# Optimization experiments

Hardware: AMD Instinct MI355X
Metric: run time of the kernel (lower is better)

## Reference

```python
import jax, jax.numpy as jnp
import numpy as np

SEQ, B, V, D, H, R = 256, 64, 10000, 1024, 1024, 2


def setup_inputs() -> dict:
    key = jax.random.key(0)
    ks = jax.random.split(key, 8)
    s = 0.02
    return {
        "tokens": jax.random.randint(ks[0], (SEQ, B), 0, V),           # (seq, batch)
        "emb": jax.random.uniform(ks[1], (V, D), minval=-0.1, maxval=0.1),
        "qw": jax.random.normal(ks[2], (R, D, H)) * s,   # Qw: nhid -> ninp, per mogrify iter
        "qb": jnp.zeros((R, D)),
        "rw": jax.random.normal(ks[3], (R, H, D)) * s,   # Rw: ninp -> nhid
        "rb": jnp.zeros((R, H)),
        "w_ih": jax.random.normal(ks[4], (4 * H, D)) * s,
        "w_hh": jax.random.normal(ks[5], (4 * H, H)) * s,
        "b_ih": jnp.zeros((4 * H,)),
        "b_hh": jnp.zeros((4 * H,)),
        "dec_w": jax.random.uniform(ks[6], (V, H), minval=-0.1, maxval=0.1),
        "dec_b": jnp.zeros((V,)),
        "h0": jnp.zeros((B, H)),
        "c0": jnp.zeros((B, H)),
    }


def reference(tokens, emb, qw, qb, rw, rb, w_ih, w_hh, b_ih, b_hh, dec_w, dec_b, h0, c0):
    def step(carry, tok):
        h, c = carry                      # (B, H), (B, H)
        x = emb[tok]                      # embedding lookup -> (B, D)
        # Mogrify: R alternating gating iterations (dropout=0 / eval mode)
        for r_ in range(R):
            x = 2.0 * jax.nn.sigmoid(h @ qw[r_].T + qb[r_]) * x   # (B, D)
            h = 2.0 * jax.nn.sigmoid(x @ rw[r_].T + rb[r_]) * h   # (B, H)
        # single-layer LSTM cell (PyTorch gate order: i, f, g, o)
        gates = x @ w_ih.T + b_ih + h @ w_hh.T + b_hh              # (B, 4H)
        i, f, g, o = jnp.split(gates, 4, axis=-1)
        c_new = jax.nn.sigmoid(f) * c + jax.nn.sigmoid(i) * jnp.tanh(g)
        h_new = jax.nn.sigmoid(o) * jnp.tanh(c_new)
        dec = h_new @ dec_w.T + dec_b                              # (B, V)
        return (h_new, c_new), dec

    (h_f, c_f), decoded = jax.lax.scan(step, (h0, c0), tokens)     # decoded: (SEQ, B, V)
    return decoded, h_f, c_f
```

## Files before the change

kernel.cpp:

```cpp
#include <hip/hip_runtime.h>
#include <hip/hip_bf16.h>

#define SEQ_LEN 256
#define NB 64
#define NV 10000
#define NVP 10048
#define ND 1024
#define NBLK 256

typedef unsigned int u32;
typedef unsigned short u16;
typedef u32 u32x4 __attribute__((ext_vector_type(4)));
typedef short s16x8 __attribute__((ext_vector_type(8)));
typedef float f32x4 __attribute__((ext_vector_type(4)));

__device__ __forceinline__ float sigf(float z) { return 1.f / (1.f + expf(-z)); }

__device__ __forceinline__ float bflo(u32 u) {
  union { u32 i; float f; } v; v.i = u << 16; return v.f;
}
__device__ __forceinline__ float bfhi(u32 u) {
  union { u32 i; float f; } v; v.i = u & 0xffff0000u; return v.f;
}
__device__ __forceinline__ u16 f2bf(float f) {
  u32 u = __float_as_uint(f);
  u32 r = u + 0x7FFFu + ((u >> 16) & 1u);
  return (u16)(r >> 16);
}

__device__ __forceinline__ void st_uc1(u32* p, u32 v) {
  asm volatile("global_store_dword %0, %1, off sc1" :: "v"(p), "v"(v) : "memory");
}
__device__ __forceinline__ void ld_a4_issue(const u32* p, u32x4& a0, u32x4& a1,
                                            u32x4& a2, u32x4& a3) {
  asm volatile(
      "global_load_dwordx4 %0, %4, off sc1\n\t"
      "global_load_dwordx4 %1, %4, off offset:64 sc1\n\t"
      "global_load_dwordx4 %2, %4, off offset:128 sc1\n\t"
      "global_load_dwordx4 %3, %4, off offset:192 sc1"
      : "=&v"(a0), "=&v"(a1), "=&v"(a2), "=&v"(a3)
      : "v"(p)
      : "memory");
}
__device__ __forceinline__ void wait_vm0() {
  asm volatile("s_waitcnt vmcnt(0)" ::: "memory");
  __builtin_amdgcn_sched_barrier(0);
}
__device__ __forceinline__ s16x8 as_frag(u32x4 v) {
  union { u32x4 u; s16x8 s; } c; c.u = v; return c.s;
}

__device__ __forceinline__ float dot8_f32(const float* hv, const float* wp, float acc) {
  float4 w0 = *(const float4*)wp;
  float4 w1 = *(const float4*)(wp + 4);
  acc += hv[0] * w0.x; acc += hv[1] * w0.y; acc += hv[2] * w0.z; acc += hv[3] * w0.w;
  acc += hv[4] * w1.x; acc += hv[5] * w1.y; acc += hv[6] * w1.z; acc += hv[7] * w1.w;
  return acc;
}

__global__ void floodk(float* out, float val, unsigned long long n) {
  unsigned long long i = (unsigned long long)blockIdx.x * 256 + threadIdx.x;
  if (i < n) out[i] = val;
}

__global__ void init_state(const float* __restrict__ h0, const float* __restrict__ c0,
                           float* __restrict__ cS, u16* __restrict__ hx16, u32* flags) {
  int i = blockIdx.x * 256 + threadIdx.x;
  int k = i >> 6, b = i & 63;
  cS[i] = c0[b * ND + k];
  hx16[b * ND + k] = f2bf(h0[b * ND + k]);
  if (i < NBLK) flags[i] = 0u;
}

__global__ void cvt_dec(const float* __restrict__ decw, u16* __restrict__ Wb) {
  size_t i = (size_t)blockIdx.x * 256 + threadIdx.x;
  size_t base = i * 8;
  if (base >= (size_t)NVP * ND) return;
  size_t row = base >> 10;
  ushort4 o0, o1;
  if (row < NV) {
    float4 v0 = *(const float4*)(decw + base);
    float4 v1 = *(const float4*)(decw + base + 4);
    o0 = make_ushort4(f2bf(v0.x), f2bf(v0.y), f2bf(v0.z), f2bf(v0.w));
    o1 = make_ushort4(f2bf(v1.x), f2bf(v1.y), f2bf(v1.z), f2bf(v1.w));
  } else {
    o0 = make_ushort4(0, 0, 0, 0); o1 = o0;
  }
  *(ushort4*)(Wb + base) = o0;
  *(ushort4*)(Wb + base + 4) = o1;
}


__device__ __forceinline__ void fbar(u32* flags, u32 want) {
  asm volatile("s_waitcnt vmcnt(0)" ::: "memory");
  __syncthreads();
  const int tid = threadIdx.x;
  if (tid == 0)
    __hip_atomic_store(flags + blockIdx.x, want,
                       __ATOMIC_RELAXED, __HIP_MEMORY_SCOPE_AGENT);
  if (tid < 64) {
    const u32* fp = flags + tid * 4;
    for (;;) {
      u32x4 f;
      asm volatile("global_load_dwordx4 %0, %1, off sc1\n\ts_waitcnt vmcnt(0)"
                   : "=&v"(f) : "v"(fp) : "memory");
      int ok = (f[0] >= want) & (f[1] >= want) & (f[2] >= want) & (f[3] >= want);
      if (__all(ok)) break;
      __builtin_amdgcn_s_sleep(1);
    }
  }
  __syncthreads();
}

template<bool EMB>
__device__ __forceinline__ void mogP(
    const u32* __restrict__ actU, const u16* wAll, int rowbase, const float* bL,
    const float* __restrict__ emb, const int* __restrict__ tok,
    const u32* __restrict__ multU, u32* __restrict__ outU,
    float* red, float* vals2, float* vals)
{
  const int tid = threadIdx.x;
  const int wv = tid >> 6, lane = tid & 63;
  const int c0 = blockIdx.x * 4;
  const int kb = wv * 128;
  const int lm = lane & 15, lh = lane >> 4;
  const u32* ap = actU + (size_t)lm * 512 + (kb >> 1) + lh * 4;
  const int g = rowbase + lm;
  const int swz = (g & 7) << 3;

  u32x4 A[4][4];
#pragma unroll
  for (int m = 0; m < 4; ++m)
    ld_a4_issue(ap + m * 8192, A[m][0], A[m][1], A[m][2], A[m][3]);
  u32 mu = 0;
  if (!EMB && tid < 256) {
    const int ec = tid >> 6, eb = tid & 63;
    const u32* mp = multU + (size_t)eb * 512 + ((c0 + ec) >> 1);
    asm volatile("global_load_dword %0, %1, off sc1" : "=&v"(mu) : "v"(mp) : "memory");
  }
  s16x8 bf[4];
#pragma unroll
  for (int ks = 0; ks < 4; ++ks)
    bf[ks] = *(const s16x8*)(wAll + g * 1024 + ((kb + ks * 32 + lh * 8) ^ swz));
  wait_vm0();

  f32x4 acc[4];
#pragma unroll
  for (int m = 0; m < 4; ++m) { acc[m] = (f32x4){0.f,0.f,0.f,0.f}; }
#pragma unroll
  for (int ks = 0; ks < 4; ++ks)
#pragma unroll
    for (int m = 0; m < 4; ++m)
      acc[m] = __builtin_amdgcn_mfma_f32_16x16x32_bf16(as_frag(A[m][ks]), bf[ks], acc[m], 0, 0, 0);

#pragma unroll
  for (int m = 0; m < 4; ++m)
#pragma unroll
    for (int r = 0; r < 4; ++r)
      red[wv * 1024 + (m * 4 + r) * 64 + lane] = acc[m][r];
  __syncthreads();
  {
    float s0 = 0.f, s1 = 0.f;
#pragma unroll
    for (int w = 0; w < 8; ++w) { s0 += red[w * 1024 + tid]; s1 += red[w * 1024 + 512 + tid]; }
    vals2[tid] = s0; vals2[512 + tid] = s1;
  }
  __syncthreads();

  if (tid < 256) {
    const int c = tid >> 6, b = tid & 63;
    const int i = ((b >> 4) << 2) | (b & 3);
    const int l = (((b >> 2) & 3) << 4) | c;
    float z = vals2[i * 64 + l] + bL[c];
    float g2 = 2.f * sigf(z);
    float m;
    if (EMB) m = emb[(size_t)tok[b] * ND + (c0 + c)];
    else     m = (c & 1) ? bfhi(mu) : bflo(mu);
    vals[c * 64 + b] = g2 * m;
  }
  __syncthreads();

  if (tid < 128) {
    const int cp = tid >> 6, b = tid & 63;
    float lo = vals[(2 * cp) * 64 + b];
    float hi = vals[(2 * cp + 1) * 64 + b];
    u32 pk = (u32)f2bf(lo) | ((u32)f2bf(hi) << 16);
    st_uc1(outU + (size_t)b * 512 + (c0 >> 1) + cp, pk);
  }
}

__device__ __forceinline__ void gatesP(
    const u32* __restrict__ xU, const u32* __restrict__ hU,
    const u16* wAll, const float* bG, float& creg,
    u32* __restrict__ hBrow, u32* __restrict__ hxU, float* __restrict__ hFw,
    float* red, float* vals2, float* vals)
{
  const int tid = threadIdx.x;
  const int wv = tid >> 6, lane = tid & 63;
  const int j0 = blockIdx.x * 4;
  const int half = wv >> 2, kq = wv & 3;
  const int kb = kq * 256;
  const int lm = lane & 15, lh = lane >> 4;
  const u32* ap = (half ? hU : xU) + (size_t)lm * 512 + (kb >> 1) + lh * 4;
  const int g = 16 + half * 16 + lm;
  const int swz = (g & 7) << 3;

  u32x4 A[4][8];
#pragma unroll
  for (int m = 0; m < 4; ++m) {
    ld_a4_issue(ap + m * 8192,      A[m][0], A[m][1], A[m][2], A[m][3]);
    ld_a4_issue(ap + m * 8192 + 64, A[m][4], A[m][5], A[m][6], A[m][7]);
  }
  s16x8 bf[8];
#pragma unroll
  for (int ks = 0; ks < 8; ++ks)
    bf[ks] = *(const s16x8*)(wAll + g * 1024 + ((kb + ks * 32 + lh * 8) ^ swz));
  wait_vm0();

  f32x4 acc[4];
#pragma unroll
  for (int m = 0; m < 4; ++m) { acc[m] = (f32x4){0.f,0.f,0.f,0.f}; }
#pragma unroll
  for (int ks = 0; ks < 8; ++ks)
#pragma unroll
    for (int m = 0; m < 4; ++m)
      acc[m] = __builtin_amdgcn_mfma_f32_16x16x32_bf16(as_frag(A[m][ks]), bf[ks], acc[m], 0, 0, 0);

#pragma unroll
  for (int m = 0; m < 4; ++m)
#pragma unroll
    for (int r = 0; r < 4; ++r)
      red[wv * 1024 + (m * 4 + r) * 64 + lane] = acc[m][r];
  __syncthreads();
  {
    float s0 = 0.f, s1 = 0.f;
#pragma unroll
    for (int w = 0; w < 8; ++w) { s0 += red[w * 1024 + tid]; s1 += red[w * 1024 + 512 + tid]; }
    vals2[tid] = s0; vals2[512 + tid] = s1;
  }
  __syncthreads();

  if (tid < 256) {
    const int jj = tid >> 6, b = tid & 63;
    const int i = ((b >> 4) << 2) | (b & 3);
    const int lbase = (((b >> 2) & 3) << 4);
    float pre[4];
#pragma unroll
    for (int gg = 0; gg < 4; ++gg) {
      const int n = jj * 4 + gg;
      pre[gg] = vals2[i * 64 + (lbase | n)] + bG[n];
    }
    float iv = sigf(pre[0]), fv = sigf(pre[1]);
    float gv = tanhf(pre[2]), ov = sigf(pre[3]);
    float cn = fv * creg + iv * gv;
    creg = cn;
    float hn = ov * tanhf(cn);
    vals[jj * 64 + b] = hn;
    if (hFw) hFw[(size_t)(j0 + jj) * NB + b] = hn;
  }
  __syncthreads();

  if (tid < 128) {
    const int cp = tid >> 6, b = tid & 63;
    float lo = vals[(2 * cp) * 64 + b];
    float hi = vals[(2 * cp + 1) * 64 + b];
    u32 pk = (u32)f2bf(lo) | ((u32)f2bf(hi) << 16);
    st_uc1(hxU + (size_t)b * 512 + (blockIdx.x * 2) + cp, pk);
    hBrow[(size_t)b * 512 + (blockIdx.x * 2) + cp] = pk;
  }
}

__global__ __launch_bounds__(512) void seq_kernel(
    const int* __restrict__ tokens, const float* __restrict__ emb,
    const float* __restrict__ qw, const float* __restrict__ qb,
    const float* __restrict__ rw, const float* __restrict__ rb,
    const float* __restrict__ wih, const float* __restrict__ whh,
    const float* __restrict__ bih, const float* __restrict__ bhh,
    u32* __restrict__ hxU, u32* __restrict__ xAU, u32* __restrict__ h1U,
    u32* __restrict__ xBU, u32* __restrict__ h3U,
    float* __restrict__ cS, u32* __restrict__ hB, float* __restrict__ hF,
    u32* flags)
{
  __shared__ u16 wAll[48 * 1024];
  __shared__ float red[8 * 1024];
  __shared__ float vals2[1024];
  __shared__ float vals[256];
  __shared__ float bMog[4][4];
  __shared__ float bGs[16];

  const int tid = threadIdx.x;
  const int c0 = blockIdx.x * 4;
  const size_t DH = (size_t)ND * ND;

  {
    const float* msrc[4] = {qw, rw, qw + DH, rw + DH};
#pragma unroll
    for (int m = 0; m < 4; ++m)
      for (int c = 0; c < 4; ++c) {
        const int g = m * 4 + c;
        const float* src = msrc[m] + (size_t)(c0 + c) * ND;
        u16* dst = wAll + g * 1024;
        const int swz = (g & 7) << 3;
        for (int k = tid; k < ND; k += 512) dst[k ^ swz] = f2bf(src[k]);
      }
#pragma unroll
    for (int m = 0; m < 2; ++m) {
      const float* W = m ? whh : wih;
      for (int r = 0; r < 16; ++r) {
        const int g = 16 + m * 16 + r;
        const float* src = W + ((size_t)(r & 3) * ND + c0 + (r >> 2)) * ND;
        u16* dst = wAll + g * 1024;
        const int swz = (g & 7) << 3;
        for (int k = tid; k < ND; k += 512) dst[k ^ swz] = f2bf(src[k]);
      }
    }
    if (tid < 16) {
      int p = tid >> 2, c = tid & 3;
      const float* bs = (p == 0) ? qb : (p == 1) ? rb : (p == 2) ? qb + ND : rb + ND;
      bMog[p][c] = bs[c0 + c];
    }
    if (tid >= 16 && tid < 32) {
      int r = tid - 16;
      int jj = r >> 2, g = r & 3;
      bGs[r] = bih[g * ND + c0 + jj] + bhh[g * ND + c0 + jj];
    }
  }
  float creg = 0.f;
  if (tid < 256) creg = cS[(size_t)(c0 + (tid >> 6)) * NB + (tid & 63)];
  __syncthreads();

  u32 want = 0;
  for (int t = 0; t < SEQ_LEN; ++t) {
    const int* tok = tokens + (size_t)t * NB;
    u32* hBrow = hB + (size_t)t * 32768;
    float* hFw = (t == SEQ_LEN - 1) ? hF : nullptr;
    mogP<true >(hxU, wAll, 0,  bMog[0], emb, tok, nullptr, xAU, red, vals2, vals); fbar(flags, ++want);
    mogP<false>(xAU, wAll, 4,  bMog[1], nullptr, nullptr, hxU, h1U, red, vals2, vals); fbar(flags, ++want);
    mogP<false>(h1U, wAll, 8,  bMog[2], nullptr, nullptr, xAU, xBU, red, vals2, vals); fbar(flags, ++want);
    mogP<false>(xBU, wAll, 12, bMog[3], nullptr, nullptr, h1U, h3U, red, vals2, vals); fbar(flags, ++want);
    gatesP(xBU, h3U, wAll, bGs, creg, hBrow, hxU, hFw, red, vals2, vals);              fbar(flags, ++want);
  }
  if (tid < 256) cS[(size_t)(c0 + (tid >> 6)) * NB + (tid & 63)] = creg;
}

__global__ __launch_bounds__(256) void decode_mfma(
    const u32* __restrict__ hB,
    const u16* __restrict__ Wb,
    const float* __restrict__ bias,
    float* __restrict__ out)
{
  int bid = blockIdx.x;
  bid = (bid & 7) * (NBLK * 157 / 8) + (bid >> 3);
  const int mt = bid / 157;
  const int nt = bid % 157;
  const int tid = threadIdx.x;
  const int wv = tid >> 6, lane = tid & 63;
  const int lm = lane & 15, lh = lane >> 4;
  const int n = nt * 64 + wv * 16 + lm;
  const u16* bp = Wb + (size_t)n * 1024 + lh * 8;
  const u32* ap = hB + (size_t)mt * 32768 + (size_t)lm * 512 + lh * 4;

  f32x4 acc[4];
#pragma unroll
  for (int m = 0; m < 4; ++m) acc[m] = (f32x4){0.f, 0.f, 0.f, 0.f};

#pragma unroll 4
  for (int ks = 0; ks < 32; ++ks) {
    s16x8 bf = *(const s16x8*)(bp + ks * 32);
#pragma unroll
    for (int m = 0; m < 4; ++m) {
      u32x4 av = *(const u32x4*)(ap + m * 8192 + ks * 16);
      acc[m] = __builtin_amdgcn_mfma_f32_16x16x32_bf16(as_frag(av), bf, acc[m], 0, 0, 0);
    }
  }

  const float db = (n < NV) ? bias[n] : 0.f;
  float* orow = out + (size_t)mt * NB * NV + n;
  if (n < NV) {
#pragma unroll
    for (int m = 0; m < 4; ++m)
#pragma unroll
      for (int r = 0; r < 4; ++r) {
        const int b = m * 16 + lh * 4 + r;
        orow[(size_t)b * NV] = acc[m][r] + db;
      }
  }
}

__global__ void finalize(const float* __restrict__ hT, const float* __restrict__ cT,
                         float* __restrict__ out) {
  int i = blockIdx.x * 256 + threadIdx.x;
  int k = i >> 6, b = i & 63;
  size_t base = (size_t)SEQ_LEN * NB * NV;
  out[base + (size_t)b * ND + k] = hT[i];
  out[base + (size_t)NB * ND + (size_t)b * ND + k] = cT[i];
}


__global__ void init_state_fb(const float* __restrict__ h0, const float* __restrict__ c0,
                              float* __restrict__ hT, float* __restrict__ cT) {
  int i = blockIdx.x * 256 + threadIdx.x;
  int k = i >> 6, b = i & 63;
  hT[i] = h0[b * ND + k];
  cT[i] = c0[b * ND + k];
}

template<bool EMB>
__global__ __launch_bounds__(256) void mog_phase(
    const float* __restrict__ actT, const float* __restrict__ W,
    const float* __restrict__ bias, const float* __restrict__ multT,
    const float* __restrict__ emb, const int* __restrict__ tok,
    float* __restrict__ outT)
{
  const int tid = threadIdx.x;
  const int wv = tid >> 6;
  const int lane = tid & 63;
  const int c0 = blockIdx.x * 4;
  __shared__ float red[4][4][64];

  float acc[4] = {0.f, 0.f, 0.f, 0.f};
  const int kb = wv * 256;
  const float* ap = actT + (size_t)kb * NB + lane;

  for (int k = 0; k < 256; k += 8) {
    float hv[8];
#pragma unroll
    for (int q = 0; q < 8; ++q) hv[q] = ap[(k + q) * NB];
#pragma unroll
    for (int c = 0; c < 4; ++c)
      acc[c] = dot8_f32(hv, W + (size_t)(c0 + c) * ND + kb + k, acc[c]);
  }
#pragma unroll
  for (int c = 0; c < 4; ++c) red[wv][c][lane] = acc[c];
  __syncthreads();

  const int c = tid >> 6, b = tid & 63;
  float z = red[0][c][b] + red[1][c][b] + red[2][c][b] + red[3][c][b];
  z += bias[c0 + c];
  float g = 2.f * sigf(z);
  float m;
  if (EMB) m = emb[(size_t)tok[b] * ND + (c0 + c)];
  else     m = multT[(size_t)(c0 + c) * NB + b];
  outT[(size_t)(c0 + c) * NB + b] = g * m;
}

__global__ __launch_bounds__(256) void lstm_gates2(
    const float* __restrict__ xT, const float* __restrict__ hT,
    const float* __restrict__ Wih, const float* __restrict__ Whh,
    const float* __restrict__ bih, const float* __restrict__ bhh,
    float* __restrict__ cT, float* __restrict__ hOut)
{
  const int tid = threadIdx.x;
  const int wv = tid >> 6, lane = tid & 63;
  const int j0 = blockIdx.x * 2;
  __shared__ float red[4][16][64];
  float acc[16];
#pragma unroll
  for (int i = 0; i < 16; ++i) acc[i] = 0.f;
  const int kb = wv * 256;
  const float* xp = xT + (size_t)kb * NB + lane;
  const float* hp = hT + (size_t)kb * NB + lane;

  for (int k = 0; k < 256; k += 8) {
    float xv[8], hv[8];
#pragma unroll
    for (int q = 0; q < 8; ++q) { xv[q] = xp[(k + q) * NB]; hv[q] = hp[(k + q) * NB]; }
#pragma unroll
    for (int jj = 0; jj < 2; ++jj)
#pragma unroll
      for (int g = 0; g < 4; ++g) {
        const size_t row = (size_t)(g * ND + j0 + jj) * ND + kb + k;
        acc[jj * 8 + g]     = dot8_f32(xv, Wih + row, acc[jj * 8 + g]);
        acc[jj * 8 + 4 + g] = dot8_f32(hv, Whh + row, acc[jj * 8 + 4 + g]);
      }
  }
#pragma unroll
  for (int i = 0; i < 16; ++i) red[wv][i][lane] = acc[i];
  __syncthreads();

  if (tid < 128) {
    const int b = tid & 63, jj = tid >> 6;
    const int j = j0 + jj;
    float pre[4];
#pragma unroll
    for (int g = 0; g < 4; ++g) {
      float s = 0.f;
#pragma unroll
      for (int w = 0; w < 4; ++w) s += red[w][jj * 8 + g][b] + red[w][jj * 8 + 4 + g][b];
      pre[g] = s + bih[g * ND + j] + bhh[g * ND + j];
    }
    float iv = sigf(pre[0]), fv = sigf(pre[1]);
    float gv = tanhf(pre[2]), ov = sigf(pre[3]);
    float cn = fv * cT[(size_t)j * NB + b] + iv * gv;
    float hn = ov * tanhf(cn);
    cT[(size_t)j * NB + b] = cn;
    hOut[(size_t)j * NB + b] = hn;
  }
}

__global__ __launch_bounds__(256) void decode_k(
    const float* __restrict__ hT, const float* __restrict__ W,
    const float* __restrict__ decb, float* __restrict__ out)
{
  const int tid = threadIdx.x;
  const int wv = tid >> 6, lane = tid & 63;
  const int v0 = blockIdx.x * 4;
  __shared__ float red[4][4][64];
  float acc[4] = {0.f, 0.f, 0.f, 0.f};
  const int kb = wv * 256;
  const float* hp = hT + (size_t)kb * NB + lane;

  for (int k = 0; k < 256; k += 8) {
    float hv[8];
#pragma unroll
    for (int q = 0; q < 8; ++q) hv[q] = hp[(k + q) * NB];
#pragma unroll
    for (int c = 0; c < 4; ++c)
      acc[c] = dot8_f32(hv, W + (size_t)(v0 + c) * ND + kb + k, acc[c]);
  }
#pragma unroll
  for (int c = 0; c < 4; ++c) red[wv][c][lane] = acc[c];
  __syncthreads();

  const int c = tid >> 6, b = tid & 63;
  float z = red[0][c][b] + red[1][c][b] + red[2][c][b] + red[3][c][b];
  z += decb[v0 + c];
  out[(size_t)b * NV + v0 + c] = z;
}

extern "C" void kernel_launch(void* const* d_in, const int* in_sizes, int n_in,
                              void* d_out, int out_size, void* d_ws, size_t ws_size,
                              hipStream_t stream)
{
  float* out = (float*)d_out;
  const unsigned long long expect_out = (unsigned long long)SEQ_LEN * NB * NV + 2ull * NB * ND;

  auto flood = [&](float v) {
    unsigned long long n = (unsigned long long)out_size;
    unsigned int g = (unsigned int)((n + 255) / 256);
    floodk<<<g, 256, 0, stream>>>(out, v, n);
  };
  const int expect_sz[14] = {
    SEQ_LEN * NB, NV * ND, 2 * ND * ND, 2 * ND, 2 * ND * ND, 2 * ND,
    4 * ND * ND, 4 * ND * ND, 4 * ND, 4 * ND, NV * ND, NV, NB * ND, NB * ND };
  if (n_in != 14) { flood(1000.f); return; }
  for (int i = 0; i < 14; ++i)
    if (in_sizes[i] != expect_sz[i]) { flood(1100.f + 100.f * i); return; }
  if ((unsigned long long)out_size != expect_out) { flood(2500.f); return; }

  float* ws = (float*)d_ws;
  const size_t SB = (size_t)ND * NB;
  if (ws_size < 7 * SB * sizeof(float)) { flood(2600.f); return; }

  const int*   tokens = (const int*)d_in[0];
  const float* emb  = (const float*)d_in[1];
  const float* qw   = (const float*)d_in[2];
  const float* qb   = (const float*)d_in[3];
  const float* rw   = (const float*)d_in[4];
  const float* rb   = (const float*)d_in[5];
  const float* wih  = (const float*)d_in[6];
  const float* whh  = (const float*)d_in[7];
  const float* bih  = (const float*)d_in[8];
  const float* bhh  = (const float*)d_in[9];
  const float* decw = (const float*)d_in[10];
  const float* decb = (const float*)d_in[11];
  const float* h0   = (const float*)d_in[12];
  const float* c0   = (const float*)d_in[13];

  float* cS    = ws;
  float* hF    = ws + SB;
  u32*   hB    = (u32*)(ws + 2 * SB);
  u16*   decwB = (u16*)(hB + (size_t)SEQ_LEN * 32768);
  u32*   ex    = (u32*)(decwB + (size_t)NVP * ND);
  const size_t EXB = 64 * 512;
  u32* hxU = ex + 0 * EXB;
  u32* xAU = ex + 1 * EXB;
  u32* h1U = ex + 2 * EXB;
  u32* xBU = ex + 3 * EXB;
  u32* h3U = ex + 4 * EXB;
  u32* flags = ex + 5 * EXB;

  const size_t DH = (size_t)ND * ND;
  const size_t need = 2 * SB * sizeof(float)
                    + (size_t)SEQ_LEN * 32768 * sizeof(u32)
                    + (size_t)NVP * ND * sizeof(u16)
                    + (5 * EXB + NBLK) * sizeof(u32);
  const bool big = ws_size >= need;

  if (big) {
    init_state<<<256, 256, 0, stream>>>(h0, c0, cS, (u16*)hxU, flags);
    cvt_dec<<<(NVP * ND / 8 + 255) / 256, 256, 0, stream>>>(decw, decwB);
    seq_kernel<<<NBLK, 512, 0, stream>>>(tokens, emb, qw, qb, rw, rb,
                                         wih, whh, bih, bhh,
                                         hxU, xAU, h1U, xBU, h3U,
                                         cS, hB, hF, flags);
    decode_mfma<<<NBLK * 157, 256, 0, stream>>>(hB, decwB, decb, out);
    finalize<<<256, 256, 0, stream>>>(hF, cS, out);
  } else {
    float* xA = ws + 0 * SB;
    float* xB = ws + 1 * SB;
    float* h1 = ws + 2 * SB;
    float* h3 = ws + 3 * SB;
    float* cSf = ws + 4 * SB;
    float* hA = ws + 5 * SB;
    float* hBf = ws + 6 * SB;
    init_state_fb<<<256, 256, 0, stream>>>(h0, c0, hA, cSf);
    float* hc = hA;
    float* hn = hBf;
    for (int t = 0; t < SEQ_LEN; ++t) {
      const int* tk = tokens + (size_t)t * NB;
      mog_phase<true ><<<256, 256, 0, stream>>>(hc, qw, qb, nullptr, emb, tk, xA);
      mog_phase<false><<<256, 256, 0, stream>>>(xA, rw, rb, hc, nullptr, nullptr, h1);
      mog_phase<false><<<256, 256, 0, stream>>>(h1, qw + DH, qb + ND, xA, nullptr, nullptr, xB);
      mog_phase<false><<<256, 256, 0, stream>>>(xB, rw + DH, rb + ND, h1, nullptr, nullptr, h3);
      lstm_gates2<<<512, 256, 0, stream>>>(xB, h3, wih, whh, bih, bhh, cSf, hn);
      decode_k<<<2500, 256, 0, stream>>>(hn, decw, decb, out + (size_t)t * NB * NV);
      float* tmp = hc; hc = hn; hn = tmp;
    }
    finalize<<<256, 256, 0, stream>>>(hc, cSf, out);
  }
}
```

Measured before the change: 16.14 ms.

## Pad barrier flags to separate cache lines and use atomic acquire loads

Each block's barrier flag moves to its own 64-byte slot (stride 16 words), and polling switches from one sc1 vector load per four flags to four relaxed atomic loads, followed by an acquire load. The inline-asm cache-bypassing A-operand loads and the explicit vmcnt wait are replaced by plain vector loads. The multiplier load is deferred to the epilogue, and the hF and hB stores now use sc1. This targets false sharing on the flag words and relies on correct memory ordering instead of hand-placed waits. In exchange, polling issues more loads, and plain loads may be served from stale non-coherent cache unless the acquire invalidates it.

```diff
diff --git a/kernel.cpp b/kernel.cpp
--- a/kernel.cpp
+++ b/kernel.cpp
@@ -31,21 +31,6 @@
 __device__ __forceinline__ void st_uc1(u32* p, u32 v) {
   asm volatile("global_store_dword %0, %1, off sc1" :: "v"(p), "v"(v) : "memory");
 }
-__device__ __forceinline__ void ld_a4_issue(const u32* p, u32x4& a0, u32x4& a1,
-                                            u32x4& a2, u32x4& a3) {
-  asm volatile(
-      "global_load_dwordx4 %0, %4, off sc1\n\t"
-      "global_load_dwordx4 %1, %4, off offset:64 sc1\n\t"
-      "global_load_dwordx4 %2, %4, off offset:128 sc1\n\t"
-      "global_load_dwordx4 %3, %4, off offset:192 sc1"
-      : "=&v"(a0), "=&v"(a1), "=&v"(a2), "=&v"(a3)
-      : "v"(p)
-      : "memory");
-}
-__device__ __forceinline__ void wait_vm0() {
-  asm volatile("s_waitcnt vmcnt(0)" ::: "memory");
-  __builtin_amdgcn_sched_barrier(0);
-}
 __device__ __forceinline__ s16x8 as_frag(u32x4 v) {
   union { u32x4 u; s16x8 s; } c; c.u = v; return c.s;
 }
@@ -69,7 +54,7 @@
   int k = i >> 6, b = i & 63;
   cS[i] = c0[b * ND + k];
   hx16[b * ND + k] = f2bf(h0[b * ND + k]);
-  if (i < NBLK) flags[i] = 0u;
+  if (i < NBLK * 16) flags[i] = 0u;
 }
 
 __global__ void cvt_dec(const float* __restrict__ decw, u16* __restrict__ Wb) {
@@ -96,18 +81,22 @@
   __syncthreads();
   const int tid = threadIdx.x;
   if (tid == 0)
-    __hip_atomic_store(flags + blockIdx.x, want,
+    __hip_atomic_store(flags + (size_t)blockIdx.x * 16, want,
                        __ATOMIC_RELAXED, __HIP_MEMORY_SCOPE_AGENT);
   if (tid < 64) {
-    const u32* fp = flags + tid * 4;
     for (;;) {
-      u32x4 f;
-      asm volatile("global_load_dwordx4 %0, %1, off sc1\n\ts_waitcnt vmcnt(0)"
-                   : "=&v"(f) : "v"(fp) : "memory");
-      int ok = (f[0] >= want) & (f[1] >= want) & (f[2] >= want) & (f[3] >= want);
+      int ok = 1;
+#pragma unroll
+      for (int i = 0; i < 4; ++i) {
+        u32 f = __hip_atomic_load(flags + (size_t)(tid * 4 + i) * 16,
+                                  __ATOMIC_RELAXED, __HIP_MEMORY_SCOPE_AGENT);
+        ok &= (f >= want);
+      }
       if (__all(ok)) break;
       __builtin_amdgcn_s_sleep(1);
     }
+    (void)__hip_atomic_load(flags + (size_t)blockIdx.x * 16,
+                            __ATOMIC_ACQUIRE, __HIP_MEMORY_SCOPE_AGENT);
   }
   __syncthreads();
 }
@@ -131,18 +120,13 @@
   u32x4 A[4][4];
 #pragma unroll
   for (int m = 0; m < 4; ++m)
-    ld_a4_issue(ap + m * 8192, A[m][0], A[m][1], A[m][2], A[m][3]);
-  u32 mu = 0;
-  if (!EMB && tid < 256) {
-    const int ec = tid >> 6, eb = tid & 63;
-    const u32* mp = multU + (size_t)eb * 512 + ((c0 + ec) >> 1);
-    asm volatile("global_load_dword %0, %1, off sc1" : "=&v"(mu) : "v"(mp) : "memory");
-  }
+#pragma unroll
+    for (int ks = 0; ks < 4; ++ks)
+      A[m][ks] = *(const u32x4*)(ap + m * 8192 + ks * 16);
   s16x8 bf[4];
 #pragma unroll
   for (int ks = 0; ks < 4; ++ks)
     bf[ks] = *(const s16x8*)(wAll + g * 1024 + ((kb + ks * 32 + lh * 8) ^ swz));
-  wait_vm0();
 
   f32x4 acc[4];
 #pragma unroll
@@ -174,8 +158,12 @@
     float z = vals2[i * 64 + l] + bL[c];
     float g2 = 2.f * sigf(z);
     float m;
-    if (EMB) m = emb[(size_t)tok[b] * ND + (c0 + c)];
-    else     m = (c & 1) ? bfhi(mu) : bflo(mu);
+    if (EMB) {
+      m = emb[(size_t)tok[b] * ND + (c0 + c)];
+    } else {
+      u32 mu = multU[(size_t)b * 512 + ((c0 + c) >> 1)];
+      m = (c & 1) ? bfhi(mu) : bflo(mu);
+    }
     vals[c * 64 + b] = g2 * m;
   }
   __syncthreads();
@@ -207,15 +195,14 @@
 
   u32x4 A[4][8];
 #pragma unroll
-  for (int m = 0; m < 4; ++m) {
-    ld_a4_issue(ap + m * 8192,      A[m][0], A[m][1], A[m][2], A[m][3]);
-    ld_a4_issue(ap + m * 8192 + 64, A[m][4], A[m][5], A[m][6], A[m][7]);
-  }
+  for (int m = 0; m < 4; ++m)
+#pragma unroll
+    for (int ks = 0; ks < 8; ++ks)
+      A[m][ks] = *(const u32x4*)(ap + m * 8192 + ks * 16);
   s16x8 bf[8];
 #pragma unroll
   for (int ks = 0; ks < 8; ++ks)
     bf[ks] = *(const s16x8*)(wAll + g * 1024 + ((kb + ks * 32 + lh * 8) ^ swz));
-  wait_vm0();
 
   f32x4 acc[4];
 #pragma unroll
@@ -256,7 +243,7 @@
     creg = cn;
     float hn = ov * tanhf(cn);
     vals[jj * 64 + b] = hn;
-    if (hFw) hFw[(size_t)(j0 + jj) * NB + b] = hn;
+    if (hFw) st_uc1((u32*)(hFw + (size_t)(j0 + jj) * NB + b), __float_as_uint(hn));
   }
   __syncthreads();
 
@@ -266,7 +253,7 @@
     float hi = vals[(2 * cp + 1) * 64 + b];
     u32 pk = (u32)f2bf(lo) | ((u32)f2bf(hi) << 16);
     st_uc1(hxU + (size_t)b * 512 + (blockIdx.x * 2) + cp, pk);
-    hBrow[(size_t)b * 512 + (blockIdx.x * 2) + cp] = pk;
+    st_uc1(hBrow + (size_t)b * 512 + (blockIdx.x * 2) + cp, pk);
   }
 }
 
@@ -584,7 +571,7 @@
   const size_t need = 2 * SB * sizeof(float)
                     + (size_t)SEQ_LEN * 32768 * sizeof(u32)
                     + (size_t)NVP * ND * sizeof(u16)
-                    + (5 * EXB + NBLK) * sizeof(u32);
+                    + (5 * EXB + NBLK * 16) * sizeof(u32);
   const bool big = ws_size >= need;
 
   if (big) {
```

Result: faster. 14.62 ms (-9.4%).
